# Performance work log

Measured on AMD Instinct MI355X. Metric: run time of the kernel, lower is better.

## Reference

```python
import jax, jax.numpy as jnp
import numpy as np

B = 16384
D_IN = 1024
D_OUT = 512
H1 = 4 * D_IN      # floor(layersDimentions[0]*inputDimention) = 4096
H3 = 4 * D_OUT     # floor(layersDimentions[1]*outputDimention) = 2048
H4 = 4 * D_OUT     # floor(layersDimentions[2]*outputDimention) = 2048
M = 256            # codebook size


def _linear_params(key, fan_in, fan_out):
    kw, kb = jax.random.split(key)
    bound = 1.0 / np.sqrt(fan_in)
    w = jax.random.uniform(kw, (fan_out, fan_in), jnp.float32, -bound, bound)
    b = jax.random.uniform(kb, (fan_out,), jnp.float32, -bound, bound)
    return w, b


def setup_inputs() -> dict:
    key = jax.random.key(0)
    ks = jax.random.split(key, 7)
    x = jax.random.normal(ks[0], (B, D_IN), jnp.float32)
    codebook = jnp.sort(jax.random.normal(ks[1], (M,), jnp.float32))
    w1, b1 = _linear_params(ks[2], D_IN, H1)
    w2, b2 = _linear_params(ks[3], H1, D_OUT)
    w3, b3 = _linear_params(ks[4], D_OUT, H3)
    w4, b4 = _linear_params(ks[5], H3, H4)
    w5, b5 = _linear_params(ks[6], H4, D_OUT)
    return {"x": x, "codebook": codebook,
            "w1": w1, "b1": b1, "w2": w2, "b2": b2,
            "w3": w3, "b3": b3, "w4": w4, "b4": b4,
            "w5": w5, "b5": b5}


def _quantize(x, codebook):
    # nearest codeword per scalar element: argmin_m |x - c_m|
    # x: [B, D], codebook: [M]
    d = jnp.abs(x[..., None] - codebook)          # [B, D, M]
    idx = jnp.argmin(d, axis=-1)                  # [B, D]
    return codebook[idx]


def reference(x, codebook, w1, b1, w2, b2, w3, b3, w4, b4, w5, b5):
    h = x @ w1.T + b1                # [B, H1]
    h = h @ w2.T + b2                # [B, D_OUT]
    h = _quantize(h, codebook)       # [B, D_OUT]
    h = h @ w3.T + b3                # [B, H3]
    h = h @ w4.T + b4                # [B, H4]
    return h @ w5.T + b5             # [B, D_OUT]
```

## Files before the change

kernel.cpp:

```cpp
#include <hip/hip_runtime.h>


typedef __bf16 v8bf __attribute__((ext_vector_type(8)));
typedef float  v4f  __attribute__((ext_vector_type(4)));

#define Bdim   16384
#define DIN    1024
#define DOUT   512
#define H1dim  4096
#define H3dim  2048
#define H4dim  2048

#define GLOBAL_AS __attribute__((address_space(1)))
#define LDS_AS    __attribute__((address_space(3)))

__device__ __forceinline__ void load16_to_lds(const __bf16* g, __bf16* l) {
  __builtin_amdgcn_global_load_lds((const GLOBAL_AS unsigned int*)g,
                                   (LDS_AS unsigned int*)l, 16, 0, 0);
}

__device__ __forceinline__ unsigned pack2bf(float a, float b) {
  return (unsigned)__builtin_bit_cast(unsigned short, (__bf16)a) |
         ((unsigned)__builtin_bit_cast(unsigned short, (__bf16)b) << 16);
}

__global__ void transpose_cast_kernel(const float* __restrict__ in,
                                      __bf16* __restrict__ out, int R, int C) {
  __shared__ float tile[32][33];
  const int c0 = blockIdx.x * 32, r0 = blockIdx.y * 32;
  const int t = threadIdx.x, tr = t >> 5, tc = t & 31;
#pragma unroll
  for (int i = 0; i < 4; ++i)
    tile[tr + i * 8][tc] = in[(size_t)(r0 + tr + i * 8) * C + (c0 + tc)];
  __syncthreads();
#pragma unroll
  for (int i = 0; i < 4; ++i)
    out[(size_t)(c0 + tr + i * 8) * R + (r0 + tc)] = (__bf16)tile[tc][tr + i * 8];
}

__global__ void bias_kernel(const float* __restrict__ b1, const float* __restrict__ w2,
                            const float* __restrict__ b2, const float* __restrict__ b3,
                            const __bf16* __restrict__ WtT, const float* __restrict__ b4,
                            const float* __restrict__ w5, const float* __restrict__ b5,
                            float* __restrict__ ba, float* __restrict__ bc) {
  const int wave = threadIdx.x >> 6, lane = threadIdx.x & 63;
  if (blockIdx.x < 128) {
    const int j = blockIdx.x * 4 + wave;
    float s = 0.f;
    for (int k = lane; k < H1dim; k += 64) s += b1[k] * w2[(size_t)j * H1dim + k];
#pragma unroll
    for (int off = 32; off; off >>= 1) s += __shfl_xor(s, off, 64);
    if (lane == 0) ba[j] = s + b2[j];
  } else {
    const int j = (blockIdx.x - 128) * 4 + wave;
    float s = 0.f;
    for (int k = lane; k < H4dim; k += 64)
      s += b3[k] * (float)WtT[(size_t)j * H4dim + k] + b4[k] * w5[(size_t)j * H4dim + k];
#pragma unroll
    for (int off = 32; off; off >>= 1) s += __shfl_xor(s, off, 64);
    if (lane == 0) bc[j] = s + b5[j];
  }
}

template <bool ABF16>
__global__ __launch_bounds__(256, 4)
void gemm_bt_splitk_kernel(const void* __restrict__ Ain, const __bf16* __restrict__ Bt,
                           float* __restrict__ Cpart, int M, int N, int K, int Kchunk) {
  __shared__ __bf16 As[64 * 32];
  __shared__ __bf16 Bs[64 * 32];
  const int t = threadIdx.x;
  const int m0 = blockIdx.x * 64;
  const int n0 = blockIdx.y * 64;
  const int kbeg = blockIdx.z * Kchunk;
  const int lane = t & 63, wave = t >> 6;
  const int quad = lane >> 4, l15 = lane & 15;
  const int wm = (wave & 1) * 32, wn = (wave >> 1) * 32;

  v4f acc[2][2];
#pragma unroll
  for (int i = 0; i < 2; ++i)
#pragma unroll
    for (int j = 0; j < 2; ++j) acc[i][j] = (v4f){0.f, 0.f, 0.f, 0.f};

  const int e = t * 8, r = e >> 5, c = e & 31;
  for (int k0 = kbeg; k0 < kbeg + Kchunk; k0 += 32) {
    if constexpr (ABF16) {
      const __bf16* A = (const __bf16*)Ain;
      *(int4*)&As[e] = *(const int4*)&A[(size_t)(m0 + r) * K + (k0 + c)];
    } else {
      const float* A = (const float*)Ain;
#pragma unroll
      for (int p = 0; p < 2; ++p) {
        const int idx = p * 256 + t;
        const int row = idx >> 3, col = (idx & 7) * 4;
        float4 v = *(const float4*)&A[(size_t)(m0 + row) * K + (k0 + col)];
        uint2 o;
        o.x = pack2bf(v.x, v.y);
        o.y = pack2bf(v.z, v.w);
        *(uint2*)&As[row * 32 + col] = o;
      }
    }
    *(int4*)&Bs[e] = *(const int4*)&Bt[(size_t)(n0 + r) * K + (k0 + c)];
    __syncthreads();
    v8bf af[2], bfr[2];
#pragma unroll
    for (int i = 0; i < 2; ++i) {
      af[i]  = *(const v8bf*)&As[(wm + i * 16 + l15) * 32 + quad * 8];
      bfr[i] = *(const v8bf*)&Bs[(wn + i * 16 + l15) * 32 + quad * 8];
    }
#pragma unroll
    for (int i = 0; i < 2; ++i)
#pragma unroll
      for (int j = 0; j < 2; ++j)
        acc[i][j] = __builtin_amdgcn_mfma_f32_16x16x32_bf16(af[i], bfr[j], acc[i][j], 0, 0, 0);
    __syncthreads();
  }

  float* dst = Cpart + (size_t)blockIdx.z * M * N;
#pragma unroll
  for (int i = 0; i < 2; ++i)
#pragma unroll
    for (int j = 0; j < 2; ++j)
#pragma unroll
      for (int r2 = 0; r2 < 4; ++r2) {
        const int gm = m0 + wm + i * 16 + quad * 4 + r2;
        const int gn = n0 + wn + j * 16 + l15;
        dst[(size_t)gm * N + gn] = acc[i][j][r2];
      }
}

__global__ void reduce_cast_kernel(const float* __restrict__ part,
                                   __bf16* __restrict__ out, int MN4, int S) {
  int i = blockIdx.x * blockDim.x + threadIdx.x;
  if (i >= MN4) return;
  const float4* p = reinterpret_cast<const float4*>(part);
  float4 s = p[i];
  for (int k = 1; k < S; ++k) {
    float4 v = p[(size_t)k * MN4 + i];
    s.x += v.x; s.y += v.y; s.z += v.z; s.w += v.w;
  }
  uint2 o;
  o.x = pack2bf(s.x, s.y);
  o.y = pack2bf(s.z, s.w);
  reinterpret_cast<uint2*>(out)[i] = o;
}

enum { MODE_Q = 1, MODE_OUT = 2 };

template <int MODE>
__global__ __launch_bounds__(256, 4)
void gemm_bt_kernel(const void* __restrict__ Ain, const __bf16* __restrict__ Bt,
                    void* __restrict__ Cout, const float* __restrict__ bias,
                    const float* __restrict__ codebook, int M, int N, int K) {
  __shared__ __bf16 As[128 * 32];
  __shared__ __bf16 Bs[64 * 32];
  __shared__ float cbs[256];

  const int t = threadIdx.x;
  const int m0 = blockIdx.x * 128;
  const int n0 = blockIdx.y * 64;
  if (MODE == MODE_Q) cbs[t] = codebook[t];

  const int lane = t & 63, wave = t >> 6;
  const int quad = lane >> 4, l15 = lane & 15;
  const int wm = (wave & 1) * 64, wn = (wave >> 1) * 32;

  const int srow = (lane >> 2);
  const int scol = (lane & 3) * 8;
  const __bf16* gB0 = Bt + (size_t)(n0 + 16 * wave + srow) * K + scol;
  __bf16* lB0 = &Bs[wave * 512];

  const __bf16* gA0 = nullptr;
  const __bf16* gA1 = nullptr;
  __bf16* lA0 = &As[wave * 512];
  __bf16* lA1 = &As[(wave + 4) * 512];
  if constexpr (MODE == MODE_OUT) {
    const __bf16* Ab = (const __bf16*)Ain;
    gA0 = Ab + (size_t)(m0 + 16 * wave + srow) * K + scol;
    gA1 = Ab + (size_t)(m0 + 64 + 16 * wave + srow) * K + scol;
  }
  const float* Af = (const float*)Ain;

  v4f acc[4][2];
#pragma unroll
  for (int i = 0; i < 4; ++i)
#pragma unroll
    for (int j = 0; j < 2; ++j) acc[i][j] = (v4f){0.f, 0.f, 0.f, 0.f};

  for (int k0 = 0; k0 < K; k0 += 32) {
    load16_to_lds(gB0 + k0, lB0);
    if constexpr (MODE == MODE_OUT) {
      load16_to_lds(gA0 + k0, lA0);
      load16_to_lds(gA1 + k0, lA1);
    } else {
#pragma unroll
      for (int p = 0; p < 4; ++p) {
        const int idx = p * 256 + t;
        const int row = idx >> 3, col = (idx & 7) * 4;
        float4 v = *(const float4*)&Af[(size_t)(m0 + row) * K + (k0 + col)];
        uint2 o;
        o.x = pack2bf(v.x, v.y);
        o.y = pack2bf(v.z, v.w);
        *(uint2*)&As[row * 32 + col] = o;
      }
    }
    __syncthreads();

    v8bf af[4], bfr[2];
#pragma unroll
    for (int i = 0; i < 4; ++i)
      af[i] = *(const v8bf*)&As[(wm + i * 16 + l15) * 32 + quad * 8];
#pragma unroll
    for (int j = 0; j < 2; ++j)
      bfr[j] = *(const v8bf*)&Bs[(wn + j * 16 + l15) * 32 + quad * 8];
#pragma unroll
    for (int i = 0; i < 4; ++i)
#pragma unroll
      for (int j = 0; j < 2; ++j)
        acc[i][j] = __builtin_amdgcn_mfma_f32_16x16x32_bf16(af[i], bfr[j], acc[i][j], 0, 0, 0);
    __syncthreads();
  }

#pragma unroll
  for (int i = 0; i < 4; ++i) {
#pragma unroll
    for (int j = 0; j < 2; ++j) {
#pragma unroll
      for (int r = 0; r < 4; ++r) {
        const int gm = m0 + wm + i * 16 + quad * 4 + r;
        const int gn = n0 + wn + j * 16 + l15;
        float v = acc[i][j][r];
        if constexpr (MODE == MODE_Q) {
          v += bias[gn];
          int idx = 0;
#pragma unroll
          for (int s = 128; s > 0; s >>= 1) {
            const int u = idx + s;
            if (cbs[u] <= v) idx = u;
          }
          float best = cbs[idx];
          if (idx < 255) {
            const float c1 = cbs[idx + 1];
            if (!(v - best <= c1 - v)) best = c1;
          }
          ((__bf16*)Cout)[(size_t)gm * N + gn] = (__bf16)best;
        } else {
          v += bias[gn];
          ((float*)Cout)[(size_t)gm * N + gn] = v;
        }
      }
    }
  }
}

extern "C" void kernel_launch(void* const* d_in, const int* in_sizes, int n_in,
                              void* d_out, int out_size, void* d_ws, size_t ws_size,
                              hipStream_t stream) {
  const float* x  = (const float*)d_in[0];
  const float* cb = (const float*)d_in[1];
  const float* w1 = (const float*)d_in[2];
  const float* b1 = (const float*)d_in[3];
  const float* w2 = (const float*)d_in[4];
  const float* b2 = (const float*)d_in[5];
  const float* w3 = (const float*)d_in[6];
  const float* b3 = (const float*)d_in[7];
  const float* w4 = (const float*)d_in[8];
  const float* b4 = (const float*)d_in[9];
  const float* w5 = (const float*)d_in[10];
  const float* b5 = (const float*)d_in[11];
  float* out = (float*)d_out;

  char* ws = (char*)d_ws;
  size_t off = 0;
  auto alloc = [&](size_t bytes) -> void* {
    void* p = ws + off;
    off = (off + bytes + 255) & ~(size_t)255;
    return p;
  };
  __bf16* w1T   = (__bf16*)alloc((size_t)DIN * H1dim * 2);
  __bf16* w4T   = (__bf16*)alloc((size_t)H3dim * H4dim * 2);
  __bf16* w3T   = (__bf16*)alloc((size_t)DOUT * H3dim * 2);
  __bf16* WaT   = (__bf16*)alloc((size_t)DOUT * DIN * 2);
  __bf16* WtT   = (__bf16*)alloc((size_t)DOUT * H3dim * 2);
  __bf16* WcT   = (__bf16*)alloc((size_t)DOUT * DOUT * 2);
  __bf16* q     = (__bf16*)alloc((size_t)Bdim * DOUT * 2);
  float*  ba    = (float*)alloc(DOUT * 4);
  float*  bc    = (float*)alloc(DOUT * 4);
  float*  part  = (float*)alloc((size_t)8 * DOUT * DIN * 4);

  transpose_cast_kernel<<<dim3(DIN / 32, H1dim / 32), 256, 0, stream>>>(w1, w1T, H1dim, DIN);
  transpose_cast_kernel<<<dim3(H3dim / 32, H4dim / 32), 256, 0, stream>>>(w4, w4T, H4dim, H3dim);
  transpose_cast_kernel<<<dim3(DOUT / 32, H3dim / 32), 256, 0, stream>>>(w3, w3T, H3dim, DOUT);

  gemm_bt_splitk_kernel<false><<<dim3(DOUT / 64, DIN / 64, 8), 256, 0, stream>>>(
      w2, w1T, part, DOUT, DIN, H1dim, H1dim / 8);
  reduce_cast_kernel<<<(DOUT * DIN / 4 + 255) / 256, 256, 0, stream>>>(
      part, WaT, DOUT * DIN / 4, 8);

  gemm_bt_splitk_kernel<false><<<dim3(DOUT / 64, H3dim / 64, 4), 256, 0, stream>>>(
      w5, w4T, part, DOUT, H3dim, H4dim, H4dim / 4);
  reduce_cast_kernel<<<(DOUT * H3dim / 4 + 255) / 256, 256, 0, stream>>>(
      part, WtT, DOUT * H3dim / 4, 4);

  bias_kernel<<<256, 256, 0, stream>>>(b1, w2, b2, b3, WtT, b4, w5, b5, ba, bc);

  gemm_bt_splitk_kernel<true><<<dim3(DOUT / 64, DOUT / 64, 8), 256, 0, stream>>>(
      WtT, w3T, part, DOUT, DOUT, H3dim, H3dim / 8);
  reduce_cast_kernel<<<(DOUT * DOUT / 4 + 255) / 256, 256, 0, stream>>>(
      part, WcT, DOUT * DOUT / 4, 8);

  gemm_bt_kernel<MODE_Q><<<dim3(Bdim / 128, DOUT / 64), 256, 0, stream>>>(
      x, WaT, q, ba, cb, Bdim, DOUT, DIN);
  gemm_bt_kernel<MODE_OUT><<<dim3(Bdim / 128, DOUT / 64), 256, 0, stream>>>(
      q, WcT, out, bc, nullptr, Bdim, DOUT, DOUT);
}
```

Baseline: 305.9 us.

## Merge prep and fold launches, pre-cast x to bf16, swizzle LDS tiles

Collapses eleven launches into six by packing independent work into shared grids: the weight transposes join an x-to-bf16 cast, the two weight folds share one grid, the two reductions share one, the third fold shares a grid with the bias kernel, and the WcT reduction rides along with the quantize GEMM. Because x is pre-cast to bf16, the quantize GEMM can use direct global-to-LDS loads. An XOR/rotate swizzle is added to the LDS layout to cut bank conflicts on MFMA fragment reads. In exchange, the extra x_bf buffer costs a full read and write pass over x, and the quantize GEMM's grid now depends on the WcT reduction blocks.

New measurement: 318.1 us. 4.0% more time.

```diff
diff --git a/kernel.cpp b/kernel.cpp
--- a/kernel.cpp
+++ b/kernel.cpp
@@ -24,54 +24,59 @@
          ((unsigned)__builtin_bit_cast(unsigned short, (__bf16)b) << 16);
 }
 
-__global__ void transpose_cast_kernel(const float* __restrict__ in,
-                                      __bf16* __restrict__ out, int R, int C) {
+__device__ __forceinline__ int swz(int m, int g) {
+  return m * 32 + ((((g + (m >> 2)) ^ (m & 3)) & 3) << 3);
+}
+
+__global__ __launch_bounds__(256)
+void prep_kernel(const float* __restrict__ x, __bf16* __restrict__ x_bf,
+                 const float* __restrict__ w1, __bf16* __restrict__ w1T,
+                 const float* __restrict__ w4, __bf16* __restrict__ w4T,
+                 const float* __restrict__ w3, __bf16* __restrict__ w3T) {
+  const int b = blockIdx.x, t = threadIdx.x;
+  if (b < 16384) {
+    const int i = b * 256 + t;
+    float4 v = reinterpret_cast<const float4*>(x)[i];
+    uint2 o;
+    o.x = pack2bf(v.x, v.y);
+    o.y = pack2bf(v.z, v.w);
+    reinterpret_cast<uint2*>(x_bf)[i] = o;
+    return;
+  }
   __shared__ float tile[32][33];
-  const int c0 = blockIdx.x * 32, r0 = blockIdx.y * 32;
-  const int t = threadIdx.x, tr = t >> 5, tc = t & 31;
+  const float* in;
+  __bf16* outp;
+  int R, C, bx, by;
+  if (b < 16384 + 4096) {
+    const int bb = b - 16384;
+    in = w1; outp = w1T; R = H1dim; C = DIN; bx = bb & 31; by = bb >> 5;
+  } else if (b < 16384 + 8192) {
+    const int bb = b - 20480;
+    in = w4; outp = w4T; R = H4dim; C = H3dim; bx = bb & 63; by = bb >> 6;
+  } else {
+    const int bb = b - 24576;
+    in = w3; outp = w3T; R = H3dim; C = DOUT; bx = bb & 15; by = bb >> 4;
+  }
+  const int c0 = bx * 32, r0 = by * 32;
+  const int tr = t >> 5, tc = t & 31;
 #pragma unroll
   for (int i = 0; i < 4; ++i)
     tile[tr + i * 8][tc] = in[(size_t)(r0 + tr + i * 8) * C + (c0 + tc)];
   __syncthreads();
 #pragma unroll
   for (int i = 0; i < 4; ++i)
-    out[(size_t)(c0 + tr + i * 8) * R + (r0 + tc)] = (__bf16)tile[tc][tr + i * 8];
-}
-
-__global__ void bias_kernel(const float* __restrict__ b1, const float* __restrict__ w2,
-                            const float* __restrict__ b2, const float* __restrict__ b3,
-                            const __bf16* __restrict__ WtT, const float* __restrict__ b4,
-                            const float* __restrict__ w5, const float* __restrict__ b5,
-                            float* __restrict__ ba, float* __restrict__ bc) {
-  const int wave = threadIdx.x >> 6, lane = threadIdx.x & 63;
-  if (blockIdx.x < 128) {
-    const int j = blockIdx.x * 4 + wave;
-    float s = 0.f;
-    for (int k = lane; k < H1dim; k += 64) s += b1[k] * w2[(size_t)j * H1dim + k];
-#pragma unroll
-    for (int off = 32; off; off >>= 1) s += __shfl_xor(s, off, 64);
-    if (lane == 0) ba[j] = s + b2[j];
-  } else {
-    const int j = (blockIdx.x - 128) * 4 + wave;
-    float s = 0.f;
-    for (int k = lane; k < H4dim; k += 64)
-      s += b3[k] * (float)WtT[(size_t)j * H4dim + k] + b4[k] * w5[(size_t)j * H4dim + k];
-#pragma unroll
-    for (int off = 32; off; off >>= 1) s += __shfl_xor(s, off, 64);
-    if (lane == 0) bc[j] = s + b5[j];
-  }
+    outp[(size_t)(c0 + tr + i * 8) * R + (r0 + tc)] = (__bf16)tile[tc][tr + i * 8];
 }
 
 template <bool ABF16>
-__global__ __launch_bounds__(256, 4)
-void gemm_bt_splitk_kernel(const void* __restrict__ Ain, const __bf16* __restrict__ Bt,
-                           float* __restrict__ Cpart, int M, int N, int K, int Kchunk) {
-  __shared__ __bf16 As[64 * 32];
-  __shared__ __bf16 Bs[64 * 32];
+__device__ __forceinline__ void fold_body(const void* __restrict__ Ain,
+                                          const __bf16* __restrict__ Bt,
+                                          float* __restrict__ Cpart,
+                                          int M, int N, int K, int Kchunk,
+                                          int bx, int by, int bz,
+                                          __bf16* As, __bf16* Bs) {
   const int t = threadIdx.x;
-  const int m0 = blockIdx.x * 64;
-  const int n0 = blockIdx.y * 64;
-  const int kbeg = blockIdx.z * Kchunk;
+  const int m0 = bx * 64, n0 = by * 64, kbeg = bz * Kchunk;
   const int lane = t & 63, wave = t >> 6;
   const int quad = lane >> 4, l15 = lane & 15;
   const int wm = (wave & 1) * 32, wn = (wave >> 1) * 32;
@@ -82,31 +87,31 @@
 #pragma unroll
     for (int j = 0; j < 2; ++j) acc[i][j] = (v4f){0.f, 0.f, 0.f, 0.f};
 
-  const int e = t * 8, r = e >> 5, c = e & 31;
+  const int r = t >> 2, cg = t & 3;
   for (int k0 = kbeg; k0 < kbeg + Kchunk; k0 += 32) {
     if constexpr (ABF16) {
       const __bf16* A = (const __bf16*)Ain;
-      *(int4*)&As[e] = *(const int4*)&A[(size_t)(m0 + r) * K + (k0 + c)];
+      *(int4*)&As[swz(r, cg)] = *(const int4*)&A[(size_t)(m0 + r) * K + k0 + cg * 8];
     } else {
       const float* A = (const float*)Ain;
 #pragma unroll
-      for (int p = 0; p < 2; ++p) {
-        const int idx = p * 256 + t;
-        const int row = idx >> 3, col = (idx & 7) * 4;
-        float4 v = *(const float4*)&A[(size_t)(m0 + row) * K + (k0 + col)];
+      for (int p2 = 0; p2 < 2; ++p2) {
+        const int idx = p2 * 256 + t;
+        const int row = idx >> 3, half = idx & 1, gg = (idx & 7) >> 1;
+        float4 v = *(const float4*)&A[(size_t)(m0 + row) * K + k0 + (idx & 7) * 4];
         uint2 o;
         o.x = pack2bf(v.x, v.y);
         o.y = pack2bf(v.z, v.w);
-        *(uint2*)&As[row * 32 + col] = o;
+        *(uint2*)&As[swz(row, gg) + half * 4] = o;
       }
     }
-    *(int4*)&Bs[e] = *(const int4*)&Bt[(size_t)(n0 + r) * K + (k0 + c)];
+    *(int4*)&Bs[swz(r, cg)] = *(const int4*)&Bt[(size_t)(n0 + r) * K + k0 + cg * 8];
     __syncthreads();
     v8bf af[2], bfr[2];
 #pragma unroll
     for (int i = 0; i < 2; ++i) {
-      af[i]  = *(const v8bf*)&As[(wm + i * 16 + l15) * 32 + quad * 8];
-      bfr[i] = *(const v8bf*)&Bs[(wn + i * 16 + l15) * 32 + quad * 8];
+      af[i]  = *(const v8bf*)&As[swz(wm + i * 16 + l15, quad)];
+      bfr[i] = *(const v8bf*)&Bs[swz(wn + i * 16 + l15, quad)];
     }
 #pragma unroll
     for (int i = 0; i < 2; ++i)
@@ -116,7 +121,7 @@
     __syncthreads();
   }
 
-  float* dst = Cpart + (size_t)blockIdx.z * M * N;
+  float* dst = Cpart + (size_t)bz * M * N;
 #pragma unroll
   for (int i = 0; i < 2; ++i)
 #pragma unroll
@@ -129,10 +134,27 @@
       }
 }
 
-__global__ void reduce_cast_kernel(const float* __restrict__ part,
-                                   __bf16* __restrict__ out, int MN4, int S) {
-  int i = blockIdx.x * blockDim.x + threadIdx.x;
-  if (i >= MN4) return;
+__global__ __launch_bounds__(256, 4)
+void fold12_kernel(const float* __restrict__ w2, const __bf16* __restrict__ w1T,
+                   float* __restrict__ part1,
+                   const float* __restrict__ w5, const __bf16* __restrict__ w4T,
+                   float* __restrict__ part2) {
+  __shared__ __bf16 As[64 * 32];
+  __shared__ __bf16 Bs[64 * 32];
+  int b = blockIdx.x;
+  if (b < 1024) {
+    fold_body<false>(w2, w1T, part1, DOUT, DIN, H1dim, 512,
+                     b & 7, (b >> 3) & 15, b >> 7, As, Bs);
+  } else {
+    b -= 1024;
+    fold_body<false>(w5, w4T, part2, DOUT, H3dim, H4dim, 512,
+                     b & 7, (b >> 3) & 31, b >> 8, As, Bs);
+  }
+}
+
+__device__ __forceinline__ void reduce_body(const float* __restrict__ part,
+                                            __bf16* __restrict__ out,
+                                            int i, int MN4, int S) {
   const float4* p = reinterpret_cast<const float4*>(part);
   float4 s = p[i];
   for (int k = 1; k < S; ++k) {
@@ -145,41 +167,77 @@
   reinterpret_cast<uint2*>(out)[i] = o;
 }
 
+__global__ __launch_bounds__(256)
+void reduce12_kernel(const float* __restrict__ part1, __bf16* __restrict__ WaT,
+                     const float* __restrict__ part2, __bf16* __restrict__ WtT) {
+  const int b = blockIdx.x, t = threadIdx.x;
+  if (b < 512) reduce_body(part1, WaT, b * 256 + t, 131072, 8);
+  else         reduce_body(part2, WtT, (b - 512) * 256 + t, 262144, 4);
+}
+
+__global__ __launch_bounds__(256, 4)
+void fold3bias_kernel(const __bf16* __restrict__ WtT, const __bf16* __restrict__ w3T,
+                      float* __restrict__ part1,
+                      const float* __restrict__ b1, const float* __restrict__ w2,
+                      const float* __restrict__ b2, const float* __restrict__ b3,
+                      const float* __restrict__ b4, const float* __restrict__ w5,
+                      const float* __restrict__ b5,
+                      float* __restrict__ ba, float* __restrict__ bc) {
+  __shared__ __bf16 As[64 * 32];
+  __shared__ __bf16 Bs[64 * 32];
+  int b = blockIdx.x;
+  if (b < 512) {
+    fold_body<true>(WtT, w3T, part1, DOUT, DOUT, H3dim, 256,
+                    b & 7, (b >> 3) & 7, b >> 6, As, Bs);
+    return;
+  }
+  b -= 512;
+  const int wave = threadIdx.x >> 6, lane = threadIdx.x & 63;
+  if (b < 128) {
+    const int j = b * 4 + wave;
+    float s = 0.f;
+    for (int k = lane; k < H1dim; k += 64) s += b1[k] * w2[(size_t)j * H1dim + k];
+#pragma unroll
+    for (int off = 32; off; off >>= 1) s += __shfl_xor(s, off, 64);
+    if (lane == 0) ba[j] = s + b2[j];
+  } else {
+    const int j = (b - 128) * 4 + wave;
+    float s = 0.f;
+    for (int k = lane; k < H4dim; k += 64)
+      s += b3[k] * (float)WtT[(size_t)j * H4dim + k] + b4[k] * w5[(size_t)j * H4dim + k];
+#pragma unroll
+    for (int off = 32; off; off >>= 1) s += __shfl_xor(s, off, 64);
+    if (lane == 0) bc[j] = s + b5[j];
+  }
+}
+
 enum { MODE_Q = 1, MODE_OUT = 2 };
 
 template <int MODE>
-__global__ __launch_bounds__(256, 4)
-void gemm_bt_kernel(const void* __restrict__ Ain, const __bf16* __restrict__ Bt,
-                    void* __restrict__ Cout, const float* __restrict__ bias,
-                    const float* __restrict__ codebook, int M, int N, int K) {
-  __shared__ __bf16 As[128 * 32];
-  __shared__ __bf16 Bs[64 * 32];
-  __shared__ float cbs[256];
-
+__device__ __forceinline__ void gemm_main(const __bf16* __restrict__ A,
+                                          const __bf16* __restrict__ Bt,
+                                          void* __restrict__ Cout,
+                                          const float* __restrict__ bias,
+                                          const float* __restrict__ codebook,
+                                          int K, int N, int mb, int nb,
+                                          __bf16* As, __bf16* Bs, float* cbs) {
   const int t = threadIdx.x;
-  const int m0 = blockIdx.x * 128;
-  const int n0 = blockIdx.y * 64;
-  if (MODE == MODE_Q) cbs[t] = codebook[t];
+  const int m0 = mb * 128, n0 = nb * 64;
+  if constexpr (MODE == MODE_Q) cbs[t] = codebook[t];
 
   const int lane = t & 63, wave = t >> 6;
   const int quad = lane >> 4, l15 = lane & 15;
   const int wm = (wave & 1) * 64, wn = (wave >> 1) * 32;
 
-  const int srow = (lane >> 2);
-  const int scol = (lane & 3) * 8;
-  const __bf16* gB0 = Bt + (size_t)(n0 + 16 * wave + srow) * K + scol;
-  __bf16* lB0 = &Bs[wave * 512];
-
-  const __bf16* gA0 = nullptr;
-  const __bf16* gA1 = nullptr;
+  const int lrow = lane >> 2;
+  const int g = (((lane & 3) ^ (lrow & 3)) - (lrow >> 2)) & 3;
+  const int scol = g * 8;
+  const __bf16* gA0 = A + (size_t)(m0 + 16 * wave + lrow) * K + scol;
+  const __bf16* gA1 = A + (size_t)(m0 + 64 + 16 * wave + lrow) * K + scol;
+  const __bf16* gB0 = Bt + (size_t)(n0 + 16 * wave + lrow) * K + scol;
   __bf16* lA0 = &As[wave * 512];
   __bf16* lA1 = &As[(wave + 4) * 512];
-  if constexpr (MODE == MODE_OUT) {
-    const __bf16* Ab = (const __bf16*)Ain;
-    gA0 = Ab + (size_t)(m0 + 16 * wave + srow) * K + scol;
-    gA1 = Ab + (size_t)(m0 + 64 + 16 * wave + srow) * K + scol;
-  }
-  const float* Af = (const float*)Ain;
+  __bf16* lB0 = &Bs[wave * 512];
 
   v4f acc[4][2];
 #pragma unroll
@@ -189,30 +247,17 @@
 
   for (int k0 = 0; k0 < K; k0 += 32) {
     load16_to_lds(gB0 + k0, lB0);
-    if constexpr (MODE == MODE_OUT) {
-      load16_to_lds(gA0 + k0, lA0);
-      load16_to_lds(gA1 + k0, lA1);
-    } else {
-#pragma unroll
-      for (int p = 0; p < 4; ++p) {
-        const int idx = p * 256 + t;
-        const int row = idx >> 3, col = (idx & 7) * 4;
-        float4 v = *(const float4*)&Af[(size_t)(m0 + row) * K + (k0 + col)];
-        uint2 o;
-        o.x = pack2bf(v.x, v.y);
-        o.y = pack2bf(v.z, v.w);
-        *(uint2*)&As[row * 32 + col] = o;
-      }
-    }
+    load16_to_lds(gA0 + k0, lA0);
+    load16_to_lds(gA1 + k0, lA1);
     __syncthreads();
 
     v8bf af[4], bfr[2];
 #pragma unroll
     for (int i = 0; i < 4; ++i)
-      af[i] = *(const v8bf*)&As[(wm + i * 16 + l15) * 32 + quad * 8];
+      af[i] = *(const v8bf*)&As[swz(wm + i * 16 + l15, quad)];
 #pragma unroll
     for (int j = 0; j < 2; ++j)
-      bfr[j] = *(const v8bf*)&Bs[(wn + j * 16 + l15) * 32 + quad * 8];
+      bfr[j] = *(const v8bf*)&Bs[swz(wn + j * 16 + l15, quad)];
 #pragma unroll
     for (int i = 0; i < 4; ++i)
 #pragma unroll
@@ -253,6 +298,31 @@
   }
 }
 
+__global__ __launch_bounds__(256, 4)
+void gemmq_kernel(const __bf16* __restrict__ x_bf, const __bf16* __restrict__ WaT,
+                  __bf16* __restrict__ q, const float* __restrict__ ba,
+                  const float* __restrict__ cbk,
+                  const float* __restrict__ part1, __bf16* __restrict__ WcT) {
+  __shared__ __bf16 As[128 * 32];
+  __shared__ __bf16 Bs[64 * 32];
+  __shared__ float cbs[256];
+  const int b = blockIdx.x;
+  if (b < 1024) {
+    gemm_main<MODE_Q>(x_bf, WaT, q, ba, cbk, DIN, DOUT, b >> 3, b & 7, As, Bs, cbs);
+  } else {
+    reduce_body(part1, WcT, (b - 1024) * 256 + threadIdx.x, 65536, 8);
+  }
+}
+
+__global__ __launch_bounds__(256, 4)
+void gemmout_kernel(const __bf16* __restrict__ q, const __bf16* __restrict__ WcT,
+                    float* __restrict__ out, const float* __restrict__ bc) {
+  __shared__ __bf16 As[128 * 32];
+  __shared__ __bf16 Bs[64 * 32];
+  const int b = blockIdx.x;
+  gemm_main<MODE_OUT>(q, WcT, out, bc, nullptr, DOUT, DOUT, b >> 3, b & 7, As, Bs, nullptr);
+}
+
 extern "C" void kernel_launch(void* const* d_in, const int* in_sizes, int n_in,
                               void* d_out, int out_size, void* d_ws, size_t ws_size,
                               hipStream_t stream) {
@@ -277,40 +347,24 @@
     off = (off + bytes + 255) & ~(size_t)255;
     return p;
   };
+  __bf16* x_bf  = (__bf16*)alloc((size_t)Bdim * DIN * 2);
   __bf16* w1T   = (__bf16*)alloc((size_t)DIN * H1dim * 2);
   __bf16* w4T   = (__bf16*)alloc((size_t)H3dim * H4dim * 2);
   __bf16* w3T   = (__bf16*)alloc((size_t)DOUT * H3dim * 2);
   __bf16* WaT   = (__bf16*)alloc((size_t)DOUT * DIN * 2);
   __bf16* WtT   = (__bf16*)alloc((size_t)DOUT * H3dim * 2);
   __bf16* WcT   = (__bf16*)alloc((size_t)DOUT * DOUT * 2);
-  __bf16* q     = (__bf16*)alloc((size_t)Bdim * DOUT * 2);
   float*  ba    = (float*)alloc(DOUT * 4);
   float*  bc    = (float*)alloc(DOUT * 4);
-  float*  part  = (float*)alloc((size_t)8 * DOUT * DIN * 4);
-
-  transpose_cast_kernel<<<dim3(DIN / 32, H1dim / 32), 256, 0, stream>>>(w1, w1T, H1dim, DIN);
-  transpose_cast_kernel<<<dim3(H3dim / 32, H4dim / 32), 256, 0, stream>>>(w4, w4T, H4dim, H3dim);
-  transpose_cast_kernel<<<dim3(DOUT / 32, H3dim / 32), 256, 0, stream>>>(w3, w3T, H3dim, DOUT);
-
-  gemm_bt_splitk_kernel<false><<<dim3(DOUT / 64, DIN / 64, 8), 256, 0, stream>>>(
-      w2, w1T, part, DOUT, DIN, H1dim, H1dim / 8);
-  reduce_cast_kernel<<<(DOUT * DIN / 4 + 255) / 256, 256, 0, stream>>>(
-      part, WaT, DOUT * DIN / 4, 8);
-
-  gemm_bt_splitk_kernel<false><<<dim3(DOUT / 64, H3dim / 64, 4), 256, 0, stream>>>(
-      w5, w4T, part, DOUT, H3dim, H4dim, H4dim / 4);
-  reduce_cast_kernel<<<(DOUT * H3dim / 4 + 255) / 256, 256, 0, stream>>>(
-      part, WtT, DOUT * H3dim / 4, 4);
-
-  bias_kernel<<<256, 256, 0, stream>>>(b1, w2, b2, b3, WtT, b4, w5, b5, ba, bc);
-
-  gemm_bt_splitk_kernel<true><<<dim3(DOUT / 64, DOUT / 64, 8), 256, 0, stream>>>(
-      WtT, w3T, part, DOUT, DOUT, H3dim, H3dim / 8);
-  reduce_cast_kernel<<<(DOUT * DOUT / 4 + 255) / 256, 256, 0, stream>>>(
-      part, WcT, DOUT * DOUT / 4, 8);
-
-  gemm_bt_kernel<MODE_Q><<<dim3(Bdim / 128, DOUT / 64), 256, 0, stream>>>(
-      x, WaT, q, ba, cb, Bdim, DOUT, DIN);
-  gemm_bt_kernel<MODE_OUT><<<dim3(Bdim / 128, DOUT / 64), 256, 0, stream>>>(
-      q, WcT, out, bc, nullptr, Bdim, DOUT, DOUT);
-}
+  float*  part1 = (float*)alloc((size_t)8 * DOUT * DIN * 4);
+  float*  part2 = (float*)alloc((size_t)4 * DOUT * H3dim * 4);
+  __bf16* q     = (__bf16*)part2;
+
+  prep_kernel<<<25600, 256, 0, stream>>>(x, x_bf, w1, w1T, w4, w4T, w3, w3T);
+  fold12_kernel<<<2048, 256, 0, stream>>>(w2, w1T, part1, w5, w4T, part2);
+  reduce12_kernel<<<1536, 256, 0, stream>>>(part1, WaT, part2, WtT);
+  fold3bias_kernel<<<768, 256, 0, stream>>>(WtT, w3T, part1,
+                                            b1, w2, b2, b3, b4, w5, b5, ba, bc);
+  gemmq_kernel<<<1280, 256, 0, stream>>>(x_bf, WaT, q, ba, cb, part1, WcT);
+  gemmout_kernel<<<1024, 256, 0, stream>>>(q, WcT, out, bc);
+}
```
